# Kernel tuning notes

Hardware: AMD Instinct MI355X
Metric: run time of the kernel (lower is better)

Reference implementation:

```python
import jax, jax.numpy as jnp
import numpy as np

STRIDES = (8, 4, 2, 1)
EPS = 1e-12  # F.normalize default eps


def _l2norm(x):
    return x / jnp.maximum(jnp.linalg.norm(x, axis=-1, keepdims=True), EPS)


def _stage(residual, stride, iw, ib, ow, ob, cb):
    B, D, T = residual.shape
    # avg_pool1d(stride, stride)
    zp = residual.reshape(B, D, T // stride, stride).mean(-1) if stride > 1 else residual
    # in_proj: 1x1 conv  [B,D,Ts] -> [B,C,Ts]
    z_e = jnp.einsum('bdt,cd->bct', zp, iw) + ib[None, :, None]
    C = z_e.shape[1]
    enc = z_e.transpose(0, 2, 1).reshape(-1, C)           # (B*Ts, C)
    enc_n = _l2norm(enc)
    cb_n = _l2norm(cb)
    dist = (enc_n ** 2).sum(1, keepdims=True) - 2.0 * enc_n @ cb_n.T + (cb_n ** 2).sum(1)[None, :]
    indices = jnp.argmax(-dist, axis=1).reshape(B, -1)    # (B, Ts)
    z_q = cb[indices].transpose(0, 2, 1)                  # (B, C, Ts) -- unnormalized codebook lookup
    commit = ((z_e - jax.lax.stop_gradient(z_q)) ** 2).mean(axis=(1, 2))
    cbloss = ((z_q - jax.lax.stop_gradient(z_e)) ** 2).mean(axis=(1, 2))
    z_q = z_e + jax.lax.stop_gradient(z_q - z_e)          # straight-through
    z_q_out = jnp.einsum('bct,dc->bdt', z_q, ow) + ob[None, :, None]
    if stride > 1:
        z_q_out = jnp.repeat(z_q_out, stride, axis=-1)
        z_e = jnp.repeat(z_e, stride, axis=-1)
    return z_q_out, commit, cbloss, indices, z_e


def setup_inputs() -> dict:
    key = jax.random.key(0)
    ks = jax.random.split(key, 6)
    return {
        'z': jax.random.normal(ks[0], (16, 512, 4096), dtype=jnp.float32),
        'in_w': jax.random.normal(ks[1], (4, 8, 512), dtype=jnp.float32) * 0.05,
        'in_b': jax.random.normal(ks[2], (4, 8), dtype=jnp.float32) * 0.05,
        'out_w': jax.random.normal(ks[3], (4, 512, 8), dtype=jnp.float32) * 0.05,
        'out_b': jax.random.normal(ks[4], (4, 512), dtype=jnp.float32) * 0.05,
        'codebooks': jax.random.normal(ks[5], (4, 1024, 8), dtype=jnp.float32),
    }


def reference(z, in_w, in_b, out_w, out_b, codebooks):
    z_q = jnp.zeros_like(z)
    residual = z
    commitment_loss = 0.0
    codebook_loss = 0.0
    codes = []
    latents = []
    for i, s in enumerate(STRIDES):
        z_q_i, commit_i, cbloss_i, idx_i, z_e_i = _stage(
            residual, s, in_w[i], in_b[i], out_w[i], out_b[i], codebooks[i])
        z_q = z_q + z_q_i  # mask is all-True in eval with n_quantizers = n_codebooks
        residual = residual - z_q_i
        commitment_loss = commitment_loss + commit_i.mean()
        codebook_loss = codebook_loss + cbloss_i.mean()
        codes.append(idx_i)
        latents.append(z_e_i)
    latents = jnp.concatenate(latents, axis=1)  # [B, N*C, T]
    return (z_q, latents, commitment_loss, codebook_loss,
            codes[0], codes[1], codes[2], codes[3])
```

## Files before the change

kernel.cpp:

```cpp
#include <hip/hip_runtime.h>


constexpr int B = 16, D = 512, T = 4096, C = 8, K = 1024, NS = 4;

constexpr long long OUT_ZQ     = 0;
constexpr long long OUT_LAT    = 33554432LL;
constexpr long long OUT_COMMIT = OUT_LAT + 2097152LL;
constexpr long long OUT_CBL    = OUT_COMMIT + 1;
constexpr long long OUT_CODES0 = OUT_CBL + 1;

__host__ __device__ constexpr long long code_off(int j) {
    return OUT_CODES0 + (j >= 1 ? 8192 : 0) + (j >= 2 ? 16384 : 0) + (j >= 3 ? 32768 : 0);
}

constexpr long long WS_CBREC = 0;
constexpr long long WS_CN2   = 32768;
constexpr long long WS_OBS   = 36864;
constexpr long long WS_LOSS  = 37376;
constexpr long long WS_CORR  = 37384;
constexpr long long WS_P0    = 40960;
constexpr long long WS_P1    = WS_P0 + 65536;
constexpr long long WS_P2    = WS_P1 + 131072;
constexpr long long WS_P3    = WS_P2 + 262144;
constexpr long long WS_TAB   = WS_P3 + 524288;
constexpr long long WS_IDX   = WS_TAB + 49152;

__host__ __device__ constexpr long long idx_off(int s) {
    return (s >= 1 ? 8192 : 0) + (s >= 2 ? 16384 : 0) + (s >= 3 ? 32768 : 0);
}
__host__ __device__ constexpr long long pbase_of(int s) {
    return (s == 0) ? WS_P0 : (s == 1) ? WS_P1 : (s == 2) ? WS_P2 : WS_P3;
}

__global__ __launch_bounds__(256) void k_prep(
    const float* __restrict__ in_w, const float* __restrict__ out_w,
    const float* __restrict__ out_b, const float* __restrict__ cb,
    float* __restrict__ ws)
{
    int bid = blockIdx.x;
    int tid = threadIdx.x;

    if (bid < 18) {
        int t = bid * 256 + tid;
        if (t == 0) ws[WS_LOSS] = 0.f;
        if (t < NS * K) {
            const float* c = cb + (long long)t * 8;
            float cv[8];
#pragma unroll
            for (int k = 0; k < 8; k++) cv[k] = c[k];
            float n2 = 0.f;
#pragma unroll
            for (int k = 0; k < 8; k++) n2 += cv[k] * cv[k];
            float den = fmaxf(sqrtf(n2), 1e-12f);
            float cn[8];
#pragma unroll
            for (int k = 0; k < 8; k++) cn[k] = cv[k] / den;
            float cn2 = 0.f;
#pragma unroll
            for (int k = 0; k < 8; k++) cn2 = fmaf(cn[k], cn[k], cn2);
            float* r = ws + WS_CBREC + (long long)t * 8;
#pragma unroll
            for (int k = 0; k < 8; k++) r[k] = -2.0f * cn[k];
            ws[WS_CN2 + t] = cn2;
        } else if (t < NS * K + D) {
            int d = t - NS * K;
            ws[WS_OBS + d] = out_b[d] + out_b[512 + d] + out_b[1024 + d] + out_b[1536 + d];
        }
        return;
    }

    int gw = (bid - 18) * 4 + (tid >> 6);
    int lane = tid & 63;
    if (gw >= 6 * 72) return;
    int p = gw / 72, idx = gw % 72;
    int i, j;
    if (p == 0) { i = 1; j = 0; }
    else if (p < 3) { i = 2; j = p - 1; }
    else { i = 3; j = p - 3; }

    double acc = 0.0;
    if (idx < 64) {
        int ci = idx >> 3, cc = idx & 7;
        const float* wi = in_w + (long long)(i * 8 + ci) * 512;
        const float* wo = out_w + (long long)j * 4096;
#pragma unroll
        for (int k = 0; k < 8; k++) {
            int d = lane + k * 64;
            acc += (double)wi[d] * (double)wo[d * 8 + cc];
        }
    } else {
        int ci = idx - 64;
        const float* wi = in_w + (long long)(i * 8 + ci) * 512;
        const float* bo = out_b + (long long)j * 512;
#pragma unroll
        for (int k = 0; k < 8; k++) {
            int d = lane + k * 64;
            acc += (double)wi[d] * (double)bo[d];
        }
    }
#pragma unroll
    for (int off = 32; off >= 1; off >>= 1) acc += __shfl_down(acc, off);
    if (lane == 0) ((double*)(ws + WS_CORR))[p * 72 + idx] = acc;
}

__global__ __launch_bounds__(512) void k_pool_proj(
    const float* __restrict__ z, const float* __restrict__ in_w,
    const float* __restrict__ in_b, const float* __restrict__ cb,
    float* __restrict__ ws)
{
    __shared__ float smem[512 * 36];

    int tid = threadIdx.x;
    int lane = tid & 63;

    if (blockIdx.y == 32) {
        int t = blockIdx.x * 512 + tid;
        if (t < 6 * 1024) {
            int p = t >> 10, code = t & 1023;
            int j = (p == 0) ? 0 : (p < 3) ? (p - 1) : (p - 3);
            const double* M = (const double*)(ws + WS_CORR) + p * 72;
            const float* q = cb + ((long long)j * K + code) * 8;
            float qv[8];
#pragma unroll
            for (int cc = 0; cc < 8; cc++) qv[cc] = q[cc];
            float* trow = ws + WS_TAB + (long long)t * 8;
#pragma unroll
            for (int c = 0; c < 8; c++) {
                double acc = M[64 + c];
#pragma unroll
                for (int cc = 0; cc < 8; cc++) acc += M[c * 8 + cc] * (double)qv[cc];
                trow[c] = (float)acc;
            }
        }
        return;
    }

    int wv = __builtin_amdgcn_readfirstlane(tid >> 6);
    int b = blockIdx.x;
    int t0 = blockIdx.y * 128;

#pragma unroll
    for (int sc = 0; sc < 32; ++sc)
        smem[tid * 36 + sc] = in_w[sc * 512 + tid];
    __syncthreads();

    const float* zrow = z + ((long long)b * D) * T + t0 + lane * 2;

    float a3[2][8] = {};
    float a2[8]    = {};
    float a1[8]    = {};
    float a0[8]    = {};

#pragma unroll 2
    for (int dd = 0; dd < 64; dd++) {
        int d = wv * 64 + dd;
        float2 v = *(const float2*)(zrow + (long long)d * T);
        const float* wrow = smem + d * 36;
        float w0[8], w1[8], w2[8], w3[8];
        *(float4*)&w0[0] = *(const float4*)(wrow + 0);
        *(float4*)&w0[4] = *(const float4*)(wrow + 4);
        *(float4*)&w1[0] = *(const float4*)(wrow + 8);
        *(float4*)&w1[4] = *(const float4*)(wrow + 12);
        *(float4*)&w2[0] = *(const float4*)(wrow + 16);
        *(float4*)&w2[4] = *(const float4*)(wrow + 20);
        *(float4*)&w3[0] = *(const float4*)(wrow + 24);
        *(float4*)&w3[4] = *(const float4*)(wrow + 28);

        float s2 = v.x + v.y;
#pragma unroll
        for (int c = 0; c < 8; c++) {
            a3[0][c] = fmaf(w3[c], v.x, a3[0][c]);
            a3[1][c] = fmaf(w3[c], v.y, a3[1][c]);
            a2[c]    = fmaf(w2[c], s2, a2[c]);
            a1[c]    = fmaf(w1[c], s2, a1[c]);
            a0[c]    = fmaf(w0[c], s2, a0[c]);
        }
    }

    __syncthreads();

    {
        float (*red)[16][64] = (float (*)[16][64])smem;
#pragma unroll
        for (int pos = 0; pos < 2; pos++)
#pragma unroll
            for (int c = 0; c < 8; c++)
                red[wv][pos * 8 + c][lane] = a3[pos][c];
        __syncthreads();
        for (int o = tid; o < 1024; o += 512) {
            int ln = o & 63, s = o >> 6;
            float sum = 0.f;
#pragma unroll
            for (int w = 0; w < 8; w++) sum += red[w][s][ln];
            int pos = s >> 3, c = s & 7;
            int tp = t0 + ln * 2 + pos;
            ws[WS_P3 + ((long long)b * 4096 + tp) * 8 + c] = sum + in_b[3 * 8 + c];
        }
        __syncthreads();
    }

    {
        float (*red)[24][64] = (float (*)[24][64])smem;
#pragma unroll
        for (int c = 0; c < 8; c++) {
            red[wv][c][lane]      = a2[c];
            red[wv][8 + c][lane]  = a1[c];
            red[wv][16 + c][lane] = a0[c];
        }
        __syncthreads();
        for (int o = tid; o < 1536; o += 512) {
            int ln = o & 63, s = o >> 6;
            if (s < 8) {
                int c = s;
                float sum = 0.f;
#pragma unroll
                for (int w = 0; w < 8; w++) sum += red[w][s][ln];
                int tp = (t0 >> 1) + ln;
                ws[WS_P2 + ((long long)b * 2048 + tp) * 8 + c] = sum * 0.5f + in_b[2 * 8 + c];
            } else if (s < 16) {
                if (ln >= 32) continue;
                int c = s - 8;
                float sum = 0.f;
#pragma unroll
                for (int w = 0; w < 8; w++) sum += red[w][s][2 * ln] + red[w][s][2 * ln + 1];
                int tp = (t0 >> 2) + ln;
                ws[WS_P1 + ((long long)b * 1024 + tp) * 8 + c] = sum * 0.25f + in_b[8 + c];
            } else {
                if (ln >= 16) continue;
                int c = s - 16;
                float sum = 0.f;
#pragma unroll
                for (int w = 0; w < 8; w++)
#pragma unroll
                    for (int k = 0; k < 4; k++) sum += red[w][s][4 * ln + k];
                int tp = (t0 >> 3) + ln;
                ws[WS_P0 + ((long long)b * 512 + tp) * 8 + c] = sum * 0.125f + in_b[c];
            }
        }
    }
}

template <int S>
__device__ __forceinline__ void vq_stage_all(
    int tid, int lane, int w, int bid,
    const float* __restrict__ cb, float* __restrict__ ws, float* __restrict__ out,
    float* __restrict__ recl, float* __restrict__ cn2l,
    float (&e_lds)[256][8], float (&en_lds)[256][8],
    float (&sbl)[16][256], unsigned short (&sil)[16][256],
    int* __restrict__ idxl, float& loss_acc)
{
    constexpr int NV = 32 << S;
    constexpr int TS = 512 << S;
    constexpr long long PB = pbase_of(S);
    constexpr int pbase = (S == 1) ? 0 : (S == 2) ? 1 : 3;
    constexpr int VPL = (NV >= 64) ? (NV / 64) : 1;
    constexpr float LW = 1.0f / (float)(65536 << S);

    {
        const float4* rs = (const float4*)(ws + WS_CBREC + (long long)S * 8192);
        float4* rd = (float4*)recl;
        rd[tid] = rs[tid];
        rd[tid + 1024] = rs[tid + 1024];
        if (tid < 256)
            ((float4*)cn2l)[tid] = ((const float4*)(ws + WS_CN2 + (long long)S * 1024))[tid];
    }

    if (tid < NV) {
        long long gv = (long long)bid * NV + tid;
        float e[8];
        const float* P = ws + PB + gv * 8;
        *(float4*)&e[0] = *(const float4*)(P + 0);
        *(float4*)&e[4] = *(const float4*)(P + 4);

        if constexpr (S > 0) {
            double ed[8];
#pragma unroll
            for (int c = 0; c < 8; c++) ed[c] = (double)e[c];
#pragma unroll
            for (int j = 0; j < S; j++) {
                int aj = tid >> (S - j);
                int cidx = idxl[((j == 0) ? 0 : (j == 1) ? 32 : 96) + aj];
                const float* trow = ws + WS_TAB + ((long long)(pbase + j) * 1024 + cidx) * 8;
#pragma unroll
                for (int c = 0; c < 8; c++) ed[c] -= (double)trow[c];
            }
#pragma unroll
            for (int c = 0; c < 8; c++) e[c] = (float)ed[c];
        }

        float n2 = 0.f;
#pragma unroll
        for (int c = 0; c < 8; c++) n2 = fmaf(e[c], e[c], n2);
        float den = fmaxf(sqrtf(n2), 1e-12f);
        float inv = 1.0f / den;
#pragma unroll
        for (int c = 0; c < 8; c++) {
            e_lds[tid][c] = e[c];
            en_lds[tid][c] = e[c] * inv;
        }
    }
    __syncthreads();

    {
        constexpr int SREP = 8 >> S;
        constexpr int SH = 3 - S;
        long long gv0 = (long long)bid * NV;
        int b0 = (int)(gv0 >> (9 + S));
        int tp0 = (int)(gv0 & (TS - 1));
        long long lat0 = OUT_LAT + ((long long)b0 * 32 + S * 8) * T + (long long)tp0 * SREP;
        int o = tid * 2;
        int c = o >> 8, r = o & 255;
        *(float2*)(out + lat0 + (long long)c * T + r) =
            make_float2(e_lds[r >> SH][c], e_lds[(r + 1) >> SH][c]);
    }

    float en_r[VPL][8];
#pragma unroll
    for (int v = 0; v < VPL; v++) {
        int sv = (NV >= 64) ? (v * 64 + lane) : (lane & (NV - 1));
#pragma unroll
        for (int c = 0; c < 8; c++) en_r[v][c] = en_lds[sv][c];
    }
    const float* rec = recl + w * 64 * 8;
    const float* c2 = cn2l + w * 64;
    float best[VPL];
    int bi[VPL];
#pragma unroll
    for (int v = 0; v < VPL; v++) { best[v] = 3.0e38f; bi[v] = 0; }

    for (int j0 = 0; j0 < 64; j0 += 4) {
        float4 cq = *(const float4*)(c2 + j0);
        float cqa[4] = { cq.x, cq.y, cq.z, cq.w };
#pragma unroll
        for (int k = 0; k < 4; k++) {
            int jt = j0 + k;
            const float* r = rec + jt * 8;
            float rr[8];
            *(float4*)&rr[0] = *(const float4*)(r + 0);
            *(float4*)&rr[4] = *(const float4*)(r + 4);
            float acc[VPL];
#pragma unroll
            for (int v = 0; v < VPL; v++) acc[v] = cqa[k];
#pragma unroll
            for (int c = 0; c < 8; c++) {
                float rc = rr[c];
#pragma unroll
                for (int v = 0; v < VPL; v++) acc[v] = fmaf(rc, en_r[v][c], acc[v]);
            }
#pragma unroll
            for (int v = 0; v < VPL; v++)
                if (acc[v] < best[v]) { best[v] = acc[v]; bi[v] = jt; }
        }
    }

#pragma unroll
    for (int v = 0; v < VPL; v++) {
        int sv = (NV >= 64) ? (v * 64 + lane) : (lane & (NV - 1));
        sbl[w][sv] = best[v];
        sil[w][sv] = (unsigned short)(w * 64 + bi[v]);
    }
    __syncthreads();

    if (tid < NV) {
        float bd = sbl[0][tid];
        int bj = sil[0][tid];
#pragma unroll
        for (int ww = 1; ww < 16; ww++) {
            float d2 = sbl[ww][tid];
            int j2 = sil[ww][tid];
            if (d2 < bd || (d2 == bd && j2 < bj)) { bd = d2; bj = j2; }
        }
        if constexpr (S == 0) idxl[tid] = bj;
        else if constexpr (S == 1) idxl[32 + tid] = bj;
        else if constexpr (S == 2) idxl[96 + tid] = bj;

        long long gv = (long long)bid * NV + tid;
        out[code_off(S) + gv] = (float)bj;
        ((int*)ws)[WS_IDX + idx_off(S) + gv] = bj;

        const float* qc = cb + ((long long)S * K + bj) * 8;
        float l = 0.f;
#pragma unroll
        for (int c = 0; c < 8; c++) {
            float dq = e_lds[tid][c] - qc[c];
            l = fmaf(dq, dq, l);
        }
        loss_acc += l * LW;
    }
    __syncthreads();
}

__global__ __launch_bounds__(1024) void k_vq_all(
    const float* __restrict__ cb, float* __restrict__ ws, float* __restrict__ out)
{
    __shared__ float recl[1024 * 8];
    __shared__ float cn2l[1024];
    __shared__ float e_lds[256][8];
    __shared__ float en_lds[256][8];
    __shared__ float sbl[16][256];
    __shared__ unsigned short sil[16][256];
    __shared__ int idxl[224];
    __shared__ float lossw[16];

    int tid = threadIdx.x;
    int lane = tid & 63;
    int w = __builtin_amdgcn_readfirstlane(tid >> 6);
    int bid = blockIdx.x;
    float loss_acc = 0.f;

    vq_stage_all<0>(tid, lane, w, bid, cb, ws, out, recl, cn2l, e_lds, en_lds, sbl, sil, idxl, loss_acc);
    vq_stage_all<1>(tid, lane, w, bid, cb, ws, out, recl, cn2l, e_lds, en_lds, sbl, sil, idxl, loss_acc);
    vq_stage_all<2>(tid, lane, w, bid, cb, ws, out, recl, cn2l, e_lds, en_lds, sbl, sil, idxl, loss_acc);
    vq_stage_all<3>(tid, lane, w, bid, cb, ws, out, recl, cn2l, e_lds, en_lds, sbl, sil, idxl, loss_acc);

#pragma unroll
    for (int off = 32; off >= 1; off >>= 1) loss_acc += __shfl_down(loss_acc, off);
    if (lane == 0) lossw[w] = loss_acc;
    __syncthreads();
    if (tid == 0) {
        float s = 0.f;
#pragma unroll
        for (int i = 0; i < 16; i++) s += lossw[i];
        atomicAdd(ws + WS_LOSS, s);
    }
}

__global__ __launch_bounds__(256) void k_zq(
    const float* __restrict__ out_w, const float* __restrict__ cb,
    const float* __restrict__ ws, float* __restrict__ out)
{
    int tid = threadIdx.x;
    int lane = tid & 63;
    int w = __builtin_amdgcn_readfirstlane(tid >> 6);
    int bid = blockIdx.x;
    int tc   = bid & 3;
    int g    = (bid >> 2) & 63;
    int b    = bid >> 8;
    int t    = tc * 1024 + w * 256 + lane * 4;

    const int* wsi = (const int*)ws;

    float q0[8], q1[8], q2[2][8], q3[4][8];
    {
        int bj = wsi[WS_IDX + idx_off(0) + (long long)b * 512 + (t >> 3)];
        const float* Q = cb + (long long)bj * 8;
#pragma unroll
        for (int c = 0; c < 8; c++) q0[c] = Q[c];
    }
    {
        int bj = wsi[WS_IDX + idx_off(1) + (long long)b * 1024 + (t >> 2)];
        const float* Q = cb + (long long)(K + bj) * 8;
#pragma unroll
        for (int c = 0; c < 8; c++) q1[c] = Q[c];
    }
#pragma unroll
    for (int j = 0; j < 2; j++) {
        int bj = wsi[WS_IDX + idx_off(2) + (long long)b * 2048 + (t >> 1) + j];
        const float* Q = cb + (long long)(2 * K + bj) * 8;
#pragma unroll
        for (int c = 0; c < 8; c++) q2[j][c] = Q[c];
    }
#pragma unroll
    for (int j = 0; j < 4; j++) {
        int bj = wsi[WS_IDX + idx_off(3) + (long long)b * 4096 + t + j];
        const float* Q = cb + (long long)(3 * K + bj) * 8;
#pragma unroll
        for (int c = 0; c < 8; c++) q3[j][c] = Q[c];
    }

#pragma unroll 2
    for (int dl = 0; dl < 8; dl++) {
        int d = g * 8 + dl;
        const float* w0 = out_w + 0 * 4096 + d * 8;
        const float* w1 = out_w + 1 * 4096 + d * 8;
        const float* w2 = out_w + 2 * 4096 + d * 8;
        const float* w3 = out_w + 3 * 4096 + d * 8;

        float acc = ws[WS_OBS + d];
#pragma unroll
        for (int c = 0; c < 8; c++) acc = fmaf(w0[c], q0[c], acc);
#pragma unroll
        for (int c = 0; c < 8; c++) acc = fmaf(w1[c], q1[c], acc);
        float accA = acc, accB = acc;
#pragma unroll
        for (int c = 0; c < 8; c++) {
            accA = fmaf(w2[c], q2[0][c], accA);
            accB = fmaf(w2[c], q2[1][c], accB);
        }
        float r0 = accA, r1 = accA, r2 = accB, r3 = accB;
#pragma unroll
        for (int c = 0; c < 8; c++) {
            r0 = fmaf(w3[c], q3[0][c], r0);
            r1 = fmaf(w3[c], q3[1][c], r1);
            r2 = fmaf(w3[c], q3[2][c], r2);
            r3 = fmaf(w3[c], q3[3][c], r3);
        }
        float* o = out + OUT_ZQ + ((long long)b * 512 + d) * T + t;
        *(float4*)o = make_float4(r0, r1, r2, r3);
    }

    if (bid == 0 && tid == 0) {
        float L = ws[WS_LOSS];
        out[OUT_COMMIT] = L;
        out[OUT_CBL]    = L;
    }
}

extern "C" void kernel_launch(void* const* d_in, const int* in_sizes, int n_in,
                              void* d_out, int out_size, void* d_ws, size_t ws_size,
                              hipStream_t stream)
{
    const float* z     = (const float*)d_in[0];
    const float* in_w  = (const float*)d_in[1];
    const float* in_b  = (const float*)d_in[2];
    const float* out_w = (const float*)d_in[3];
    const float* out_b = (const float*)d_in[4];
    const float* cb    = (const float*)d_in[5];
    float* out = (float*)d_out;
    float* ws  = (float*)d_ws;

    k_prep<<<dim3(126), dim3(256), 0, stream>>>(in_w, out_w, out_b, cb, ws);
    k_pool_proj<<<dim3(16, 33), dim3(512), 0, stream>>>(z, in_w, in_b, cb, ws);
    k_vq_all<<<dim3(256), dim3(1024), 0, stream>>>(cb, ws, out);
    k_zq<<<dim3(4096), dim3(256), 0, stream>>>(out_w, cb, ws, out);
}
```

Before: 121.6 us.

## Fuse prep into pooling kernel, widen time tile, compute correction rows in LDS

Merges the prep kernel into the pooling/projection kernel so one launch does both, removing a kernel launch. The pooling tile is widened to four timesteps per lane using float4 loads, which halves the block count and doubles the work per block. The precomputed correction table in the workspace is dropped. Its rows are now computed on the fly inside the VQ kernel for just the selected codes and kept in LDS, which removes a global gather but adds double-precision math and shared-memory use. This relies on the fused kernel's prep blocks finishing their CORR and codebook writes before the VQ kernel reads them, which stream order guarantees.

```diff
diff --git a/kernel.cpp b/kernel.cpp
--- a/kernel.cpp
+++ b/kernel.cpp
@@ -22,8 +22,7 @@
 constexpr long long WS_P1    = WS_P0 + 65536;
 constexpr long long WS_P2    = WS_P1 + 131072;
 constexpr long long WS_P3    = WS_P2 + 262144;
-constexpr long long WS_TAB   = WS_P3 + 524288;
-constexpr long long WS_IDX   = WS_TAB + 49152;
+constexpr long long WS_IDX   = WS_P3 + 524288;
 
 __host__ __device__ constexpr long long idx_off(int s) {
     return (s >= 1 ? 8192 : 0) + (s >= 2 ? 16384 : 0) + (s >= 3 ? 32768 : 0);
@@ -32,129 +31,101 @@
     return (s == 0) ? WS_P0 : (s == 1) ? WS_P1 : (s == 2) ? WS_P2 : WS_P3;
 }
 
-__global__ __launch_bounds__(256) void k_prep(
-    const float* __restrict__ in_w, const float* __restrict__ out_w,
+__global__ __launch_bounds__(512) void k_pool_prep(
+    const float* __restrict__ z, const float* __restrict__ in_w,
+    const float* __restrict__ in_b, const float* __restrict__ out_w,
     const float* __restrict__ out_b, const float* __restrict__ cb,
     float* __restrict__ ws)
 {
+    __shared__ float smem[512 * 36];
+
     int bid = blockIdx.x;
     int tid = threadIdx.x;
-
-    if (bid < 18) {
-        int t = bid * 256 + tid;
-        if (t == 0) ws[WS_LOSS] = 0.f;
-        if (t < NS * K) {
-            const float* c = cb + (long long)t * 8;
-            float cv[8];
-#pragma unroll
-            for (int k = 0; k < 8; k++) cv[k] = c[k];
-            float n2 = 0.f;
-#pragma unroll
-            for (int k = 0; k < 8; k++) n2 += cv[k] * cv[k];
-            float den = fmaxf(sqrtf(n2), 1e-12f);
-            float cn[8];
-#pragma unroll
-            for (int k = 0; k < 8; k++) cn[k] = cv[k] / den;
-            float cn2 = 0.f;
-#pragma unroll
-            for (int k = 0; k < 8; k++) cn2 = fmaf(cn[k], cn[k], cn2);
-            float* r = ws + WS_CBREC + (long long)t * 8;
-#pragma unroll
-            for (int k = 0; k < 8; k++) r[k] = -2.0f * cn[k];
-            ws[WS_CN2 + t] = cn2;
-        } else if (t < NS * K + D) {
-            int d = t - NS * K;
-            ws[WS_OBS + d] = out_b[d] + out_b[512 + d] + out_b[1024 + d] + out_b[1536 + d];
+    int lane = tid & 63;
+
+    if (bid >= 256) {
+        if (bid < 265) {
+            int t = (bid - 256) * 512 + tid;
+            if (t == 0) ws[WS_LOSS] = 0.f;
+            if (t < NS * K) {
+                const float* c = cb + (long long)t * 8;
+                float cv[8];
+#pragma unroll
+                for (int k = 0; k < 8; k++) cv[k] = c[k];
+                float n2 = 0.f;
+#pragma unroll
+                for (int k = 0; k < 8; k++) n2 += cv[k] * cv[k];
+                float den = fmaxf(sqrtf(n2), 1e-12f);
+                float cn[8];
+#pragma unroll
+                for (int k = 0; k < 8; k++) cn[k] = cv[k] / den;
+                float cn2 = 0.f;
+#pragma unroll
+                for (int k = 0; k < 8; k++) cn2 = fmaf(cn[k], cn[k], cn2);
+                float* r = ws + WS_CBREC + (long long)t * 8;
+#pragma unroll
+                for (int k = 0; k < 8; k++) r[k] = -2.0f * cn[k];
+                ws[WS_CN2 + t] = cn2;
+            } else if (t < NS * K + D) {
+                int d = t - NS * K;
+                ws[WS_OBS + d] = out_b[d] + out_b[512 + d] + out_b[1024 + d] + out_b[1536 + d];
+            }
+        } else {
+            int gw = (bid - 265) * 8 + (tid >> 6);
+            if (gw >= 6 * 72) return;
+            int p = gw / 72, idx = gw % 72;
+            int i, j;
+            if (p == 0) { i = 1; j = 0; }
+            else if (p < 3) { i = 2; j = p - 1; }
+            else { i = 3; j = p - 3; }
+
+            double acc = 0.0;
+            if (idx < 64) {
+                int ci = idx >> 3, cc = idx & 7;
+                const float* wi = in_w + (long long)(i * 8 + ci) * 512;
+                const float* wo = out_w + (long long)j * 4096;
+#pragma unroll
+                for (int k = 0; k < 8; k++) {
+                    int d = lane + k * 64;
+                    acc += (double)wi[d] * (double)wo[d * 8 + cc];
+                }
+            } else {
+                int ci = idx - 64;
+                const float* wi = in_w + (long long)(i * 8 + ci) * 512;
+                const float* bo = out_b + (long long)j * 512;
+#pragma unroll
+                for (int k = 0; k < 8; k++) {
+                    int d = lane + k * 64;
+                    acc += (double)wi[d] * (double)bo[d];
+                }
+            }
+#pragma unroll
+            for (int off = 32; off >= 1; off >>= 1) acc += __shfl_down(acc, off);
+            if (lane == 0) ((double*)(ws + WS_CORR))[p * 72 + idx] = acc;
         }
         return;
     }
 
-    int gw = (bid - 18) * 4 + (tid >> 6);
-    int lane = tid & 63;
-    if (gw >= 6 * 72) return;
-    int p = gw / 72, idx = gw % 72;
-    int i, j;
-    if (p == 0) { i = 1; j = 0; }
-    else if (p < 3) { i = 2; j = p - 1; }
-    else { i = 3; j = p - 3; }
-
-    double acc = 0.0;
-    if (idx < 64) {
-        int ci = idx >> 3, cc = idx & 7;
-        const float* wi = in_w + (long long)(i * 8 + ci) * 512;
-        const float* wo = out_w + (long long)j * 4096;
-#pragma unroll
-        for (int k = 0; k < 8; k++) {
-            int d = lane + k * 64;
-            acc += (double)wi[d] * (double)wo[d * 8 + cc];
-        }
-    } else {
-        int ci = idx - 64;
-        const float* wi = in_w + (long long)(i * 8 + ci) * 512;
-        const float* bo = out_b + (long long)j * 512;
-#pragma unroll
-        for (int k = 0; k < 8; k++) {
-            int d = lane + k * 64;
-            acc += (double)wi[d] * (double)bo[d];
-        }
-    }
-#pragma unroll
-    for (int off = 32; off >= 1; off >>= 1) acc += __shfl_down(acc, off);
-    if (lane == 0) ((double*)(ws + WS_CORR))[p * 72 + idx] = acc;
-}
-
-__global__ __launch_bounds__(512) void k_pool_proj(
-    const float* __restrict__ z, const float* __restrict__ in_w,
-    const float* __restrict__ in_b, const float* __restrict__ cb,
-    float* __restrict__ ws)
-{
-    __shared__ float smem[512 * 36];
-
-    int tid = threadIdx.x;
-    int lane = tid & 63;
-
-    if (blockIdx.y == 32) {
-        int t = blockIdx.x * 512 + tid;
-        if (t < 6 * 1024) {
-            int p = t >> 10, code = t & 1023;
-            int j = (p == 0) ? 0 : (p < 3) ? (p - 1) : (p - 3);
-            const double* M = (const double*)(ws + WS_CORR) + p * 72;
-            const float* q = cb + ((long long)j * K + code) * 8;
-            float qv[8];
-#pragma unroll
-            for (int cc = 0; cc < 8; cc++) qv[cc] = q[cc];
-            float* trow = ws + WS_TAB + (long long)t * 8;
-#pragma unroll
-            for (int c = 0; c < 8; c++) {
-                double acc = M[64 + c];
-#pragma unroll
-                for (int cc = 0; cc < 8; cc++) acc += M[c * 8 + cc] * (double)qv[cc];
-                trow[c] = (float)acc;
-            }
-        }
-        return;
-    }
-
     int wv = __builtin_amdgcn_readfirstlane(tid >> 6);
-    int b = blockIdx.x;
-    int t0 = blockIdx.y * 128;
+    int b = bid & 15;
+    int t0 = (bid >> 4) * 256;
 
 #pragma unroll
     for (int sc = 0; sc < 32; ++sc)
         smem[tid * 36 + sc] = in_w[sc * 512 + tid];
     __syncthreads();
 
-    const float* zrow = z + ((long long)b * D) * T + t0 + lane * 2;
-
-    float a3[2][8] = {};
-    float a2[8]    = {};
+    const float* zrow = z + ((long long)b * D) * T + t0 + lane * 4;
+
+    float a3[4][8] = {};
+    float a2[2][8] = {};
     float a1[8]    = {};
     float a0[8]    = {};
 
 #pragma unroll 2
     for (int dd = 0; dd < 64; dd++) {
         int d = wv * 64 + dd;
-        float2 v = *(const float2*)(zrow + (long long)d * T);
+        float4 v = *(const float4*)(zrow + (long long)d * T);
         const float* wrow = smem + d * 36;
         float w0[8], w1[8], w2[8], w3[8];
         *(float4*)&w0[0] = *(const float4*)(wrow + 0);
@@ -166,77 +137,94 @@
         *(float4*)&w3[0] = *(const float4*)(wrow + 24);
         *(float4*)&w3[4] = *(const float4*)(wrow + 28);
 
-        float s2 = v.x + v.y;
+        float s2a = v.x + v.y, s2b = v.z + v.w;
+        float s4 = s2a + s2b;
 #pragma unroll
         for (int c = 0; c < 8; c++) {
             a3[0][c] = fmaf(w3[c], v.x, a3[0][c]);
             a3[1][c] = fmaf(w3[c], v.y, a3[1][c]);
-            a2[c]    = fmaf(w2[c], s2, a2[c]);
-            a1[c]    = fmaf(w1[c], s2, a1[c]);
-            a0[c]    = fmaf(w0[c], s2, a0[c]);
+            a3[2][c] = fmaf(w3[c], v.z, a3[2][c]);
+            a3[3][c] = fmaf(w3[c], v.w, a3[3][c]);
+            a2[0][c] = fmaf(w2[c], s2a, a2[0][c]);
+            a2[1][c] = fmaf(w2[c], s2b, a2[1][c]);
+            a1[c]    = fmaf(w1[c], s4, a1[c]);
+            a0[c]    = fmaf(w0[c], s4, a0[c]);
         }
     }
 
     __syncthreads();
 
     {
-        float (*red)[16][64] = (float (*)[16][64])smem;
-#pragma unroll
-        for (int pos = 0; pos < 2; pos++)
+        float (*red)[32][64] = (float (*)[32][64])smem;
+#pragma unroll
+        for (int pos = 0; pos < 4; pos++)
 #pragma unroll
             for (int c = 0; c < 8; c++)
                 red[wv][pos * 8 + c][lane] = a3[pos][c];
         __syncthreads();
-        for (int o = tid; o < 1024; o += 512) {
+        for (int o = tid; o < 2048; o += 512) {
             int ln = o & 63, s = o >> 6;
             float sum = 0.f;
 #pragma unroll
             for (int w = 0; w < 8; w++) sum += red[w][s][ln];
             int pos = s >> 3, c = s & 7;
-            int tp = t0 + ln * 2 + pos;
+            int tp = t0 + ln * 4 + pos;
             ws[WS_P3 + ((long long)b * 4096 + tp) * 8 + c] = sum + in_b[3 * 8 + c];
         }
         __syncthreads();
     }
 
     {
-        float (*red)[24][64] = (float (*)[24][64])smem;
+        float (*red)[32][64] = (float (*)[32][64])smem;
+#pragma unroll
+        for (int pos = 0; pos < 2; pos++)
+#pragma unroll
+            for (int c = 0; c < 8; c++)
+                red[wv][pos * 8 + c][lane] = a2[pos][c];
 #pragma unroll
         for (int c = 0; c < 8; c++) {
-            red[wv][c][lane]      = a2[c];
-            red[wv][8 + c][lane]  = a1[c];
-            red[wv][16 + c][lane] = a0[c];
+            red[wv][16 + c][lane] = a1[c];
+            red[wv][24 + c][lane] = a0[c];
         }
         __syncthreads();
-        for (int o = tid; o < 1536; o += 512) {
+        for (int o = tid; o < 2048; o += 512) {
             int ln = o & 63, s = o >> 6;
-            if (s < 8) {
-                int c = s;
+            if (s < 16) {
                 float sum = 0.f;
 #pragma unroll
                 for (int w = 0; w < 8; w++) sum += red[w][s][ln];
-                int tp = (t0 >> 1) + ln;
+                int pos = s >> 3, c = s & 7;
+                int tp = (t0 >> 1) + ln * 2 + pos;
                 ws[WS_P2 + ((long long)b * 2048 + tp) * 8 + c] = sum * 0.5f + in_b[2 * 8 + c];
-            } else if (s < 16) {
-                if (ln >= 32) continue;
-                int c = s - 8;
+            } else if (s < 24) {
+                int c = s - 16;
                 float sum = 0.f;
 #pragma unroll
-                for (int w = 0; w < 8; w++) sum += red[w][s][2 * ln] + red[w][s][2 * ln + 1];
+                for (int w = 0; w < 8; w++) sum += red[w][s][ln];
                 int tp = (t0 >> 2) + ln;
                 ws[WS_P1 + ((long long)b * 1024 + tp) * 8 + c] = sum * 0.25f + in_b[8 + c];
             } else {
-                if (ln >= 16) continue;
-                int c = s - 16;
+                if (ln & 1) continue;
+                int c = s - 24;
                 float sum = 0.f;
 #pragma unroll
-                for (int w = 0; w < 8; w++)
-#pragma unroll
-                    for (int k = 0; k < 4; k++) sum += red[w][s][4 * ln + k];
-                int tp = (t0 >> 3) + ln;
+                for (int w = 0; w < 8; w++) sum += red[w][s][ln] + red[w][s][ln + 1];
+                int tp = (t0 >> 3) + (ln >> 1);
                 ws[WS_P0 + ((long long)b * 512 + tp) * 8 + c] = sum * 0.125f + in_b[c];
             }
         }
+    }
+}
+
+__device__ __forceinline__ void corr_row(
+    const double* __restrict__ M, const float* __restrict__ q, float* __restrict__ dst)
+{
+#pragma unroll
+    for (int c = 0; c < 8; c++) {
+        double acc = M[64 + c];
+#pragma unroll
+        for (int cc = 0; cc < 8; cc++) acc += M[c * 8 + cc] * (double)q[cc];
+        dst[c] = (float)acc;
     }
 }
 
@@ -247,7 +235,7 @@
     float* __restrict__ recl, float* __restrict__ cn2l,
     float (&e_lds)[256][8], float (&en_lds)[256][8],
     float (&sbl)[16][256], unsigned short (&sil)[16][256],
-    int* __restrict__ idxl, float& loss_acc)
+    int* __restrict__ idxl, float (&ltab)[352][8], float& loss_acc)
 {
     constexpr int NV = 32 << S;
     constexpr int TS = 512 << S;
@@ -255,6 +243,7 @@
     constexpr int pbase = (S == 1) ? 0 : (S == 2) ? 1 : 3;
     constexpr int VPL = (NV >= 64) ? (NV / 64) : 1;
     constexpr float LW = 1.0f / (float)(65536 << S);
+    constexpr int PBARR[6] = { 0, 32, 64, 128, 160, 224 };
 
     {
         const float4* rs = (const float4*)(ws + WS_CBREC + (long long)S * 8192);
@@ -278,9 +267,7 @@
             for (int c = 0; c < 8; c++) ed[c] = (double)e[c];
 #pragma unroll
             for (int j = 0; j < S; j++) {
-                int aj = tid >> (S - j);
-                int cidx = idxl[((j == 0) ? 0 : (j == 1) ? 32 : 96) + aj];
-                const float* trow = ws + WS_TAB + ((long long)(pbase + j) * 1024 + cidx) * 8;
+                const float* trow = ltab[PBARR[pbase + j] + (tid >> (S - j))];
 #pragma unroll
                 for (int c = 0; c < 8; c++) ed[c] -= (double)trow[c];
             }
@@ -379,13 +366,29 @@
         ((int*)ws)[WS_IDX + idx_off(S) + gv] = bj;
 
         const float* qc = cb + ((long long)S * K + bj) * 8;
+        float qv[8];
+#pragma unroll
+        for (int c = 0; c < 8; c++) qv[c] = qc[c];
+
         float l = 0.f;
 #pragma unroll
         for (int c = 0; c < 8; c++) {
-            float dq = e_lds[tid][c] - qc[c];
+            float dq = e_lds[tid][c] - qv[c];
             l = fmaf(dq, dq, l);
         }
         loss_acc += l * LW;
+
+        const double* corrd = (const double*)(ws + WS_CORR);
+        if constexpr (S == 0) {
+            corr_row(corrd + 0 * 72, qv, ltab[0 + tid]);
+            corr_row(corrd + 1 * 72, qv, ltab[32 + tid]);
+            corr_row(corrd + 3 * 72, qv, ltab[128 + tid]);
+        } else if constexpr (S == 1) {
+            corr_row(corrd + 2 * 72, qv, ltab[64 + tid]);
+            corr_row(corrd + 4 * 72, qv, ltab[160 + tid]);
+        } else if constexpr (S == 2) {
+            corr_row(corrd + 5 * 72, qv, ltab[224 + tid]);
+        }
     }
     __syncthreads();
 }
@@ -400,6 +403,7 @@
     __shared__ float sbl[16][256];
     __shared__ unsigned short sil[16][256];
     __shared__ int idxl[224];
+    __shared__ float ltab[352][8];
     __shared__ float lossw[16];
 
     int tid = threadIdx.x;
@@ -408,10 +412,10 @@
     int bid = blockIdx.x;
     float loss_acc = 0.f;
 
-    vq_stage_all<0>(tid, lane, w, bid, cb, ws, out, recl, cn2l, e_lds, en_lds, sbl, sil, idxl, loss_acc);
-    vq_stage_all<1>(tid, lane, w, bid, cb, ws, out, recl, cn2l, e_lds, en_lds, sbl, sil, idxl, loss_acc);
-    vq_stage_all<2>(tid, lane, w, bid, cb, ws, out, recl, cn2l, e_lds, en_lds, sbl, sil, idxl, loss_acc);
-    vq_stage_all<3>(tid, lane, w, bid, cb, ws, out, recl, cn2l, e_lds, en_lds, sbl, sil, idxl, loss_acc);
+    vq_stage_all<0>(tid, lane, w, bid, cb, ws, out, recl, cn2l, e_lds, en_lds, sbl, sil, idxl, ltab, loss_acc);
+    vq_stage_all<1>(tid, lane, w, bid, cb, ws, out, recl, cn2l, e_lds, en_lds, sbl, sil, idxl, ltab, loss_acc);
+    vq_stage_all<2>(tid, lane, w, bid, cb, ws, out, recl, cn2l, e_lds, en_lds, sbl, sil, idxl, ltab, loss_acc);
+    vq_stage_all<3>(tid, lane, w, bid, cb, ws, out, recl, cn2l, e_lds, en_lds, sbl, sil, idxl, ltab, loss_acc);
 
 #pragma unroll
     for (int off = 32; off >= 1; off >>= 1) loss_acc += __shfl_down(loss_acc, off);
@@ -519,8 +523,7 @@
     float* out = (float*)d_out;
     float* ws  = (float*)d_ws;
 
-    k_prep<<<dim3(126), dim3(256), 0, stream>>>(in_w, out_w, out_b, cb, ws);
-    k_pool_proj<<<dim3(16, 33), dim3(512), 0, stream>>>(z, in_w, in_b, cb, ws);
+    k_pool_prep<<<dim3(319), dim3(512), 0, stream>>>(z, in_w, in_b, out_w, out_b, cb, ws);
     k_vq_all<<<dim3(256), dim3(1024), 0, stream>>>(cb, ws, out);
     k_zq<<<dim3(4096), dim3(256), 0, stream>>>(out_w, cb, ws, out);
 }
```

Result: no change. 122.9 us, median of 3 (+1.1%).
